# Kernel optimization log

Measured on AMD Instinct MI355X. Metric: run time of the kernel, lower is better.

The kernel has to match this reference:

```python
import jax, jax.numpy as jnp
import numpy as np

B, S, M = 2, 2048, 2048
NQ, NKV, H = 16, 4, 128
EPS = 1e-6
MAX_WAVELENGTH = 10000.0
NEG_INF = -1e9


def rmsnorm(x, scale, eps=EPS):
    # RMSNorm over head_dim (last axis), computed in fp32.
    xf = x.astype(jnp.float32)
    var = jnp.mean(xf * xf, axis=-1, keepdims=True)
    return (xf * jax.lax.rsqrt(var + eps) * scale).astype(x.dtype)


def rope(x, max_wavelength=MAX_WAVELENGTH, scaling_factor=1.0, start_index=0):
    # x: [b, s, n, h]; keras_hub split-half rotary embedding.
    h = x.shape[-1]
    inv_freq = 1.0 / (max_wavelength ** (jnp.arange(0, h, 2, dtype=jnp.float32) / h))
    pos = (jnp.arange(x.shape[1], dtype=jnp.float32) + start_index) / scaling_factor
    freq = pos[:, None] * inv_freq[None, :]             # [s, h/2]
    emb = jnp.concatenate([freq, freq], axis=-1)        # [s, h]
    cos = jnp.cos(emb)[None, :, None, :]
    sin = jnp.sin(emb)[None, :, None, :]
    x1, x2 = x[..., : h // 2], x[..., h // 2 :]
    rot = jnp.concatenate([-x2, x1], axis=-1)
    return (x * cos + rot * sin).astype(x.dtype)


def setup_inputs() -> dict:
    key = jax.random.key(0)
    ks = jax.random.split(key, 6)
    hidden_states = jax.random.normal(ks[0], (B, S, M), dtype=jnp.float32)
    # causal mask [b, q, k]
    causal = jnp.tril(jnp.ones((S, S), dtype=bool))
    attention_mask = jnp.broadcast_to(causal[None], (B, S, S))
    sq = 0.02
    Wq = jax.random.normal(ks[1], (M, NQ, H), dtype=jnp.float32) * sq
    Wk = jax.random.normal(ks[2], (M, NKV, H), dtype=jnp.float32) * sq
    Wv = jax.random.normal(ks[3], (M, NKV, H), dtype=jnp.float32) * sq
    Wo = jax.random.normal(ks[4], (NQ, H, M), dtype=jnp.float32) * sq
    q_scale = jnp.ones((H,), dtype=jnp.float32)
    k_scale = jnp.ones((H,), dtype=jnp.float32)
    return {
        "hidden_states": hidden_states,
        "attention_mask": attention_mask,
        "Wq": Wq,
        "Wk": Wk,
        "Wv": Wv,
        "Wo": Wo,
        "q_scale": q_scale,
        "k_scale": k_scale,
    }


def reference(hidden_states, attention_mask, Wq, Wk, Wv, Wo, q_scale, k_scale):
    inv_norm = 1.0 / np.sqrt(H)
    groups = NQ // NKV

    q = jnp.einsum("bqm,muh->bquh", hidden_states, Wq)   # [b,q,NQ,H]
    q = rope(rmsnorm(q, q_scale))
    k = jnp.einsum("bkm,mvh->bkvh", hidden_states, Wk)   # [b,k,NKV,H]
    k = rope(rmsnorm(k, k_scale))
    v = jnp.einsum("bkm,mvh->bkvh", hidden_states, Wv)

    # GQA broadcast: repeat each kv head `groups` times consecutively.
    k = jnp.repeat(k, groups, axis=2)
    v = jnp.repeat(v, groups, axis=2)

    scores = jnp.einsum("bquh,bkuh->buqk", q, k) * inv_norm  # [b,u,q,k]
    scores = scores.astype(jnp.float32)
    scores = jnp.where(attention_mask[:, None, :, :], scores, NEG_INF)
    probs = jax.nn.softmax(scores, axis=-1).astype(hidden_states.dtype)

    attn = jnp.einsum("buqk,bkuh->bquh", probs, v)
    out = jnp.einsum("bquh,uhm->bqm", attn, Wo)
    return out
```

## Files before the change

kernel.cpp:

```cpp
#include <hip/hip_runtime.h>
#include <stdint.h>

#define BB 2
#define SS 2048
#define MM 2048
#define NQ 16
#define NKV 4
#define HH 128
#define KVB 64

typedef __attribute__((ext_vector_type(4))) float f32x4;
typedef __attribute__((ext_vector_type(16))) float f32x16;
typedef _Float16 f16x8 __attribute__((ext_vector_type(8)));
typedef _Float16 f16x4 __attribute__((ext_vector_type(4)));
typedef _Float16 f16x2 __attribute__((ext_vector_type(2)));
typedef unsigned int uint4v __attribute__((ext_vector_type(4)));

__device__ __forceinline__ void gll16(const _Float16* g, _Float16* l) {
  __builtin_amdgcn_global_load_lds(
      (__attribute__((address_space(1))) void*)g,
      (__attribute__((address_space(3))) void*)l, 16, 0, 0);
}

__device__ __forceinline__ float fexp2(float x) {
#if __has_builtin(__builtin_amdgcn_exp2f)
  return __builtin_amdgcn_exp2f(x);
#else
  float r;
  asm("v_exp_f32 %0, %1" : "=v"(r) : "v"(x));
  return r;
#endif
}

__device__ __forceinline__ float fsin2pi(float rev) {
  float f, s;
  asm("v_fract_f32 %0, %1" : "=v"(f) : "v"(rev));
  asm("v_sin_f32 %0, %1" : "=v"(s) : "v"(f));
  return s;
}
__device__ __forceinline__ float fcos2pi(float rev) {
  float f, c;
  asm("v_fract_f32 %0, %1" : "=v"(f) : "v"(rev));
  asm("v_cos_f32 %0, %1" : "=v"(c) : "v"(f));
  return c;
}

__device__ __forceinline__ unsigned int pkrtz(float a, float b) {
  return __builtin_bit_cast(unsigned int, __builtin_amdgcn_cvt_pkrtz(a, b));
}

__global__ __launch_bounds__(256) void k_prep(
    const float* __restrict__ hidden,
    const float* __restrict__ Wq, const float* __restrict__ Wk,
    const float* __restrict__ Wv, const float* __restrict__ Wo,
    _Float16* __restrict__ Xb,
    _Float16* __restrict__ Wqkvt, _Float16* __restrict__ Wot) {
  const int z = blockIdx.z;
  if (z >= 4) {
    const int bid = (z - 4) * 4096 + blockIdx.y * 64 + blockIdx.x;
    const int i = bid * 256 + threadIdx.x;
    float4 v = ((const float4*)hidden)[i];
    f16x4 o = { (_Float16)v.x, (_Float16)v.y, (_Float16)v.z, (_Float16)v.w };
    ((f16x4*)Xb)[i] = o;
    return;
  }
  if (blockIdx.x >= 16) return;
  if ((z == 1 || z == 2) && blockIdx.y >= 16) return;
  const float* in = (z == 0) ? Wq : (z == 1) ? Wk : (z == 2) ? Wv : Wo;
  _Float16* out = (z == 3) ? Wot : Wqkvt;
  const int N_in = (z == 1 || z == 2) ? 512 : 2048;
  const int n_off = (z == 1) ? 2048 : (z == 2) ? 2560 : 0;

  __shared__ float tile[128][33];
  const int k0 = blockIdx.x * 128;
  const int n0 = blockIdx.y * 32;
  {
    const int rr = threadIdx.x >> 3;
    const int c4 = threadIdx.x & 7;
    #pragma unroll
    for (int it = 0; it < 4; ++it) {
      const int r = it * 32 + rr;
      const float4 v = *(const float4*)(&in[(size_t)(k0 + r) * N_in + n0 + c4 * 4]);
      tile[r][c4 * 4 + 0] = v.x;
      tile[r][c4 * 4 + 1] = v.y;
      tile[r][c4 * 4 + 2] = v.z;
      tile[r][c4 * 4 + 3] = v.w;
    }
  }
  __syncthreads();
  {
    const int rw = threadIdx.x >> 5;
    const int lk = threadIdx.x & 31;
    #pragma unroll
    for (int it = 0; it < 4; ++it) {
      const int r = it * 8 + rw;
      f16x4 o = { (_Float16)tile[lk * 4 + 0][r], (_Float16)tile[lk * 4 + 1][r],
                  (_Float16)tile[lk * 4 + 2][r], (_Float16)tile[lk * 4 + 3][r] };
      *(f16x4*)(&out[(size_t)(n0 + r + n_off) * 2048 + k0 + lk * 4]) = o;
    }
  }
}

template <int FN, bool F16OUT>
__global__ __launch_bounds__(512, 2) void k_gemm256(
    const _Float16* __restrict__ A, const _Float16* __restrict__ Bt,
    void* __restrict__ Cout, int NT_M, int N, int K) {
  __shared__ _Float16 As[2][256 * 64];
  __shared__ _Float16 Bs[2][FN * 64 * 64];

  const int tid = threadIdx.x;
  const int w = tid >> 6;
  const int l = tid & 63;
  const int lr = l & 15;
  const int al4 = l >> 4;
  const int wr = w >> 2;
  const int wc = w & 3;
  const int swz = (lr & 7) << 4;

  const int nwg = gridDim.x;
  const int bid = blockIdx.x;
  const int sbid = (bid & 7) * (nwg >> 3) + (bid >> 3);
  const int bm = (sbid % NT_M) * 256;
  const int bn = (sbid / NT_M) * (FN * 64);
  const int KT = K >> 6;

  const int srow = tid >> 3;
  const int sch = (tid & 7) ^ (srow & 7);
  const _Float16* aSrc = A + (size_t)(bm + srow) * K + sch * 8;
  const _Float16* bSrc = Bt + (size_t)(bn + srow) * K + sch * 8;

  auto stA = [&](int buf, int r, int kt) {
    gll16(aSrc + (size_t)(r * 64) * K + kt * 64, &As[buf][r * 4096 + w * 512]);
  };
  auto stB = [&](int buf, int r, int kt) {
    gll16(bSrc + (size_t)(r * 64) * K + kt * 64, &Bs[buf][r * 4096 + w * 512]);
  };

  f32x4 acc[8][FN] = {};

  stA(0, 0, 0); stA(0, 1, 0); stA(0, 2, 0); stA(0, 3, 0);
  stB(0, 0, 0); stB(0, 1, 0);
  if (FN == 3) stB(0, 2, 0);
  if (KT > 1) {
    stA(1, 0, 1); stA(1, 2, 1); stB(1, 0, 1); stB(1, 1, 1);
    asm volatile("s_waitcnt vmcnt(4)" ::: "memory");
  } else {
    asm volatile("s_waitcnt vmcnt(0)" ::: "memory");
  }
  __builtin_amdgcn_s_barrier();

  for (int t = 0; t < KT; ++t) {
    const int cb = t & 1;
    const char* Ab = (const char*)&As[cb][0];
    const char* Bb = (const char*)&Bs[cb][0];
    f16x8 bF[FN][2];
    #pragma unroll
    for (int ph = 0; ph < 2; ++ph) {
      f16x8 aF[4][2];
      #pragma unroll
      for (int fm = 0; fm < 4; ++fm)
        #pragma unroll
        for (int ks = 0; ks < 2; ++ks) {
          const int row = wr * 128 + (ph * 4 + fm) * 16 + lr;
          aF[fm][ks] = *(const f16x8*)(Ab + row * 128 + (((ks * 4 + al4) * 16) ^ swz));
        }
      if (ph == 0) {
        #pragma unroll
        for (int fn = 0; fn < FN; ++fn)
          #pragma unroll
          for (int ks = 0; ks < 2; ++ks) {
            const int col = wc * (FN * 16) + fn * 16 + lr;
            bF[fn][ks] = *(const f16x8*)(Bb + col * 128 + (((ks * 4 + al4) * 16) ^ swz));
          }
      }
      if (ph == 0 && t + 1 < KT) {
        if (FN == 3) stB(cb ^ 1, 2, t + 1);
        stA(cb ^ 1, 1, t + 1); stA(cb ^ 1, 3, t + 1);
      }
      if (ph == 1 && t + 2 < KT) {
        stA(cb, 0, t + 2); stA(cb, 2, t + 2);
        stB(cb, 0, t + 2); stB(cb, 1, t + 2);
      }
      __builtin_amdgcn_s_barrier();
      asm volatile("s_waitcnt lgkmcnt(0)" ::: "memory");
      __builtin_amdgcn_sched_barrier(0);
      __builtin_amdgcn_s_setprio(1);
      #pragma unroll
      for (int fm = 0; fm < 4; ++fm)
        #pragma unroll
        for (int fn = 0; fn < FN; ++fn)
          #pragma unroll
          for (int ks = 0; ks < 2; ++ks)
            acc[ph * 4 + fm][fn] = __builtin_amdgcn_mfma_f32_16x16x32_f16(
                aF[fm][ks], bF[fn][ks], acc[ph * 4 + fm][fn], 0, 0, 0);
      __builtin_amdgcn_s_setprio(0);
      __builtin_amdgcn_sched_barrier(0);
      if (ph == 0) {
        __builtin_amdgcn_s_barrier();
      } else {
        if (t + 2 < KT) asm volatile("s_waitcnt vmcnt(4)" ::: "memory");
        else            asm volatile("s_waitcnt vmcnt(0)" ::: "memory");
        __builtin_amdgcn_s_barrier();
      }
    }
  }

  #pragma unroll
  for (int fm = 0; fm < 8; ++fm) {
    #pragma unroll
    for (int i = 0; i < 4; ++i) {
      const int row = bm + wr * 128 + fm * 16 + al4 * 4 + i;
      #pragma unroll
      for (int fn = 0; fn < FN; ++fn) {
        const int col = bn + wc * (FN * 16) + fn * 16 + lr;
        if (F16OUT)
          ((_Float16*)Cout)[(size_t)row * N + col] = (_Float16)acc[fm][fn][i];
        else
          ((float*)Cout)[(size_t)row * N + col] = acc[fm][fn][i];
      }
    }
  }
}

__global__ __launch_bounds__(256) void k_normrope(
    const _Float16* __restrict__ qkv,
    const float* __restrict__ q_scale, const float* __restrict__ k_scale,
    _Float16* __restrict__ Qr, _Float16* __restrict__ Kr,
    _Float16* __restrict__ VtG) {
  __shared__ _Float16 vtile[32][33];
  if (blockIdx.y == 5) {
    if (blockIdx.x >= 2048) return;
    const int s0 = (blockIdx.x & 63) * 32;
    const int zz = blockIdx.x >> 6;
    const int h0 = (zz & 3) * 32;
    const int bv = zz >> 2;
    const int b = bv >> 2;
    const int hv = bv & 3;
    const int tx = threadIdx.x & 31;
    const int ty = threadIdx.x >> 5;
    #pragma unroll
    for (int r = ty; r < 32; r += 8)
      vtile[r][tx] = qkv[(size_t)(b * SS + s0 + r) * 3072 + 2560 + hv * 128 + h0 + tx];
    __syncthreads();
    #pragma unroll
    for (int r = ty; r < 32; r += 8)
      VtG[((size_t)bv * HH + h0 + r) * SS + s0 + tx] = vtile[tx][r];
    return;
  }
  const int row = blockIdx.x;
  const int b = row >> 11;
  const int s = row & 2047;
  const int hh = blockIdx.y * 4 + (threadIdx.x >> 6);
  const int l = threadIdx.x & 63;
  const _Float16* src = qkv + (size_t)row * 3072 + hh * 128 + l * 2;
  float x0 = (float)src[0];
  float x1 = (float)src[1];
  float ssum = x0 * x0 + x1 * x1;
  #pragma unroll
  for (int d = 1; d < 64; d <<= 1) ssum += __shfl_xor(ssum, d);
  const float rstd = rsqrtf(ssum * (1.f / 128.f) + 1e-6f);
  const float* scl = (hh < 16) ? q_scale : k_scale;
  x0 *= rstd * scl[2 * l];
  x1 *= rstd * scl[2 * l + 1];
  const float y0 = __shfl_xor(x0, 32);
  const float y1 = __shfl_xor(x1, 32);
  const int j0 = (2 * l) & 63;
  const float kLog = 0.20762050593046014f;
  const float inv2pi = 0.15915494309189535f;
  const float rev0 = (float)s * fexp2(-(float)j0 * kLog) * inv2pi;
  const float rev1 = (float)s * fexp2(-(float)(j0 + 1) * kLog) * inv2pi;
  const float c0 = fcos2pi(rev0), s0 = fsin2pi(rev0);
  const float c1 = fcos2pi(rev1), s1 = fsin2pi(rev1);
  float r0, r1;
  if (l < 32) { r0 = x0 * c0 - y0 * s0; r1 = x1 * c1 - y1 * s1; }
  else        { r0 = x0 * c0 + y0 * s0; r1 = x1 * c1 + y1 * s1; }
  if (hh < 16) {
    _Float16* dst = Qr + ((size_t)(b * NQ + hh) * SS + s) * HH + 2 * l;
    dst[0] = (_Float16)r0; dst[1] = (_Float16)r1;
  } else {
    _Float16* dst = Kr + ((size_t)(b * NKV + (hh - 16)) * SS + s) * HH + 2 * l;
    dst[0] = (_Float16)r0; dst[1] = (_Float16)r1;
  }
}

__device__ const unsigned char g_tasks[24] = {
  61, 63, 28,
  57, 59, 53, 55, 24,
  49, 51, 45, 47, 20,
  41, 43, 37, 39, 16,
  33, 35, 12,
  8, 4, 0
};

__global__ __launch_bounds__(256, 2) void k_attn(
    const _Float16* __restrict__ Qr, const _Float16* __restrict__ Kr,
    const _Float16* __restrict__ VtG,
    const float* __restrict__ qs, const float* __restrict__ ks,
    float* __restrict__ PartA, float* __restrict__ PartB,
    float* __restrict__ psA, float* __restrict__ psB,
    _Float16* __restrict__ Ao) {
  __shared__ _Float16 Ks[128 * 128];
  __shared__ _Float16 Vs[128 * 128];

  const int tid = threadIdx.x;
  const int w = tid >> 6;
  const int l = tid & 63;
  const int l31 = l & 31;
  const int hi = l >> 5;
  const int sw7 = (l31 & 7) << 4;

  const int n = blockIdx.y * 32 + blockIdx.x;
  const int g = n & 7;
  const int slot9 = n >> 3;
  const int j = slot9 & 3;
  const int b = g >> 2;
  const int kvh = g & 3;
  const int u = kvh * 4 + j;
  const int bu = b * 16 + u;

  const int task = g_tasks[slot9 >> 2];
  const int heavy = task & 1;
  const int half = (task >> 1) & 1;
  const int qt = task >> 2;
  const int q0 = qt * 128;
  const int total = 2 * qt + 2;
  const int h0 = ((qt + 2) >> 1) << 1;
  const int t0 = heavy ? (half ? h0 : 0) : 0;
  const int t1 = heavy ? (half ? total : h0) : total;

  float ma = fmaxf(fabsf(qs[l]), fabsf(qs[l + 64]));
  float mb = fmaxf(fabsf(ks[l]), fabsf(ks[l + 64]));
  #pragma unroll
  for (int d = 1; d < 64; d <<= 1) {
    ma = fmaxf(ma, __shfl_xor(ma, d));
    mb = fmaxf(mb, __shfl_xor(mb, d));
  }
  const float M2 = 1.4426950408889634f * ma * mb;
  const float K2 = 0.12752982260735795f;

  const _Float16* Kbase = Kr + (size_t)(b * NKV + kvh) * SS * HH;
  const _Float16* Vbase = VtG + (size_t)(b * NKV + kvh) * HH * SS;

  f16x8 qf[8];
  {
    const _Float16* qp = Qr + ((size_t)(b * NQ + u) * SS + q0 + w * 32 + l31) * HH + hi * 8;
    #pragma unroll
    for (int hs = 0; hs < 8; hs++) {
      qf[hs] = *(const f16x8*)(qp + hs * 16);
      qf[hs] *= (_Float16)K2;
    }
  }

  f32x16 acc0 = {}, acc1 = {}, acc2 = {}, acc3 = {};
  float psum = 0.f;

  auto stage = [&](int m) {
    const int kv0 = m * KVB;
    #pragma unroll
    for (int it = 0; it < 8; it++) {
      const int nn = it * 256 + tid;
      const int row = nn >> 4, c = nn & 15;
      const int cs = c ^ (row & 7);
      gll16(Kbase + (size_t)(kv0 + row) * HH + cs * 8,
            &Ks[(size_t)(it * 256 + w * 64) * 8]);
      gll16(Vbase + (size_t)row * SS + kv0 + cs * 8,
            &Vs[(size_t)(it * 256 + w * 64) * 8]);
    }
  };

  const int qwb = q0 + w * 32;
  const int qlane = qwb + l31;

  for (int m = t0; m < t1; m += 2) {
    stage(m);
    __syncthreads();
    const char* Kb = (const char*)&Ks[0];
    const char* Vb = (const char*)&Vs[0];
    #pragma unroll
    for (int hh2 = 0; hh2 < 2; ++hh2) {
      const int kv0 = m * KVB + hh2 * 64;
      if (kv0 <= qwb + 31) {
        f32x16 S0 = {}, S1 = {};
        __builtin_amdgcn_s_setprio(1);
        #pragma unroll
        for (int hs = 0; hs < 8; hs++) {
          const int ch = hs * 2 + hi;
          f16x8 k0 = *(const f16x8*)(Kb + (hh2 * 64 + l31) * 256 + ((ch << 4) ^ sw7));
          f16x8 k1 = *(const f16x8*)(Kb + (hh2 * 64 + 32 + l31) * 256 + ((ch << 4) ^ sw7));
          S0 = __builtin_amdgcn_mfma_f32_32x32x16_f16(k0, qf[hs], S0, 0, 0, 0);
          S1 = __builtin_amdgcn_mfma_f32_32x32x16_f16(k1, qf[hs], S1, 0, 0, 0);
        }
        __builtin_amdgcn_s_setprio(0);

        const bool domask = (kv0 + 63 > qwb);
        float p0[16], p1[16];
        #pragma unroll
        for (int r = 0; r < 16; r++) {
          const int cr = (r & 3) + 8 * (r >> 2) + 4 * hi;
          float e0 = fexp2(S0[r] - M2);
          float e1 = fexp2(S1[r] - M2);
          if (domask) {
            if (kv0 + cr > qlane) e0 = 0.f;
            if (kv0 + 32 + cr > qlane) e1 = 0.f;
          }
          p0[r] = e0; p1[r] = e1;
          psum += e0 + e1;
        }

        unsigned int pkv[4][4];
        #pragma unroll
        for (int gg = 0; gg < 4; gg++) {
          pkv[0][gg] = pkrtz(p0[2 * gg], p0[2 * gg + 1]);
          pkv[1][gg] = pkrtz(p0[8 + 2 * gg], p0[9 + 2 * gg]);
          pkv[2][gg] = pkrtz(p1[2 * gg], p1[2 * gg + 1]);
          pkv[3][gg] = pkrtz(p1[8 + 2 * gg], p1[9 + 2 * gg]);
        }
        f16x8 pa[4];
        #pragma unroll
        for (int ksx = 0; ksx < 4; ksx++) {
          unsigned int a0 = pkv[ksx][0], a1 = pkv[ksx][1], a2 = pkv[ksx][2], a3 = pkv[ksx][3];
          unsigned int x0 = (unsigned int)__shfl_xor((int)a0, 32);
          unsigned int x1 = (unsigned int)__shfl_xor((int)a1, 32);
          unsigned int x2 = (unsigned int)__shfl_xor((int)a2, 32);
          unsigned int x3 = (unsigned int)__shfl_xor((int)a3, 32);
          uint4v dv;
          dv.x = hi ? x2 : a0;
          dv.y = hi ? x3 : a1;
          dv.z = hi ? a2 : x0;
          dv.w = hi ? a3 : x1;
          pa[ksx] = __builtin_bit_cast(f16x8, dv);
        }

        __builtin_amdgcn_s_setprio(1);
        #pragma unroll
        for (int ksx = 0; ksx < 4; ksx++) {
          const int ch = hh2 * 8 + ksx * 2 + hi;
          f16x8 v0 = *(const f16x8*)(Vb + (0 * 32 + l31) * 256 + ((ch << 4) ^ sw7));
          acc0 = __builtin_amdgcn_mfma_f32_32x32x16_f16(pa[ksx], v0, acc0, 0, 0, 0);
          f16x8 v1 = *(const f16x8*)(Vb + (1 * 32 + l31) * 256 + ((ch << 4) ^ sw7));
          acc1 = __builtin_amdgcn_mfma_f32_32x32x16_f16(pa[ksx], v1, acc1, 0, 0, 0);
          f16x8 v2 = *(const f16x8*)(Vb + (2 * 32 + l31) * 256 + ((ch << 4) ^ sw7));
          acc2 = __builtin_amdgcn_mfma_f32_32x32x16_f16(pa[ksx], v2, acc2, 0, 0, 0);
          f16x8 v3 = *(const f16x8*)(Vb + (3 * 32 + l31) * 256 + ((ch << 4) ^ sw7));
          acc3 = __builtin_amdgcn_mfma_f32_32x32x16_f16(pa[ksx], v3, acc3, 0, 0, 0);
        }
        __builtin_amdgcn_s_setprio(0);
      }
    }
    __syncthreads();
  }

  const float tot = psum + __shfl_xor(psum, 32);
  if (heavy) {
    const int slot = bu * 8 + (qt - 8);
    float* pPart = (half ? PartB : PartA) + (size_t)slot * 16384;
    float* sPart = (half ? psB : psA) + slot * 128;
    if (hi == 0) sPart[w * 32 + l31] = tot;
    #pragma unroll
    for (int r = 0; r < 16; r++) {
      const int cr = (r & 3) + 8 * (r >> 2) + 4 * hi;
      float* dst = pPart + (size_t)(w * 32 + cr) * 128 + l31;
      dst[0]  = acc0[r];
      dst[32] = acc1[r];
      dst[64] = acc2[r];
      dst[96] = acc3[r];
    }
  } else {
    const float inv = 1.f / tot;
    #pragma unroll
    for (int r = 0; r < 16; r++) {
      const int cr = (r & 3) + 8 * (r >> 2) + 4 * hi;
      const float ivr = __shfl(inv, cr);
      _Float16* dst = Ao + ((size_t)(b * SS + q0 + w * 32 + cr)) * MM + u * HH + l31;
      dst[0]  = (_Float16)(acc0[r] * ivr);
      dst[32] = (_Float16)(acc1[r] * ivr);
      dst[64] = (_Float16)(acc2[r] * ivr);
      dst[96] = (_Float16)(acc3[r] * ivr);
    }
  }
}

__global__ __launch_bounds__(256) void k_fin(
    const float* __restrict__ PartA, const float* __restrict__ PartB,
    const float* __restrict__ psA, const float* __restrict__ psB,
    _Float16* __restrict__ Ao) {
  const int slot = blockIdx.x;
  const int bu = slot >> 3, st = slot & 7;
  const int b = bu >> 4, u = bu & 15;
  const int qt = st + 8;
  const float* pa = PartA + (size_t)slot * 16384;
  const float* pb = PartB + (size_t)slot * 16384;
  const float* sa = psA + slot * 128;
  const float* sb = psB + slot * 128;
  #pragma unroll
  for (int it = 0; it < 16; it++) {
    const int unit = it * 256 + threadIdx.x;
    const int qr = unit >> 5, cg = unit & 31;
    const float inv = 1.f / (sa[qr] + sb[qr]);
    f32x4 va = *(const f32x4*)(pa + qr * 128 + cg * 4);
    f32x4 vb = *(const f32x4*)(pb + qr * 128 + cg * 4);
    f16x4 o = { (_Float16)((va[0] + vb[0]) * inv), (_Float16)((va[1] + vb[1]) * inv),
                (_Float16)((va[2] + vb[2]) * inv), (_Float16)((va[3] + vb[3]) * inv) };
    *(f16x4*)(Ao + ((size_t)(b * SS + qt * 128 + qr)) * MM + u * HH + cg * 4) = o;
  }
}

extern "C" void kernel_launch(void* const* d_in, const int* in_sizes, int n_in,
                              void* d_out, int out_size, void* d_ws, size_t ws_size,
                              hipStream_t stream) {
  const float* hidden = (const float*)d_in[0];
  const float* Wq = (const float*)d_in[2];
  const float* Wk = (const float*)d_in[3];
  const float* Wv = (const float*)d_in[4];
  const float* Wo = (const float*)d_in[5];
  const float* q_scale = (const float*)d_in[6];
  const float* k_scale = (const float*)d_in[7];

  char* ws = (char*)d_ws;
  _Float16* Xb    = (_Float16*)(ws);
  _Float16* Wqkvt = (_Float16*)(ws + 16777216);
  _Float16* Wot   = (_Float16*)(ws + 29360128);
  _Float16* qkv   = (_Float16*)(ws + 37748736);
  _Float16* Qr    = (_Float16*)(ws + 62914560);
  _Float16* Kr    = (_Float16*)(ws + 79691776);
  _Float16* VtG   = (_Float16*)(ws + 83886080);
  _Float16* Ao    = (_Float16*)(ws + 88080384);
  float*    PartB = (float*)(ws);
  float*    PartA = (float*)(ws + 37748736);
  float*    psA   = (float*)(ws + 54525952);
  float*    psB   = (float*)(ws + 54657024);

  k_prep<<<dim3(64, 64, 6), dim3(256), 0, stream>>>(hidden, Wq, Wk, Wv, Wo, Xb, Wqkvt, Wot);
  k_gemm256<3, true><<<dim3(256), dim3(512), 0, stream>>>(Xb, Wqkvt, (void*)qkv, 16, 3072, 2048);
  k_normrope<<<dim3(4096, 6), dim3(256), 0, stream>>>(qkv, q_scale, k_scale, Qr, Kr, VtG);
  k_attn<<<dim3(32, 24), dim3(256), 0, stream>>>(Qr, Kr, VtG, q_scale, k_scale,
                                                 PartA, PartB, psA, psB, Ao);
  k_fin<<<dim3(256), dim3(256), 0, stream>>>(PartA, PartB, psA, psB, Ao);
  k_gemm256<2, false><<<dim3(256), dim3(512), 0, stream>>>(Ao, Wot, d_out, 16, 2048, 2048);
}
```

Before: 193.7 us.

## Shrink GEMM N-tile to 128, single-buffer B tile, raise occupancy target

The GEMM kernel now uses a fixed 256x128 output tile instead of the 256x192 tile used for the QKV projection, so that GEMM launches 384 blocks instead of 256. The B tile in LDS drops from double to single buffering: the next B tile is loaded in the second phase, after every wave has pulled its B fragments into registers. The launch bounds now ask for 4 blocks per CU, with vmcnt waits adjusted to match. The aim is better load balance across CUs and less LDS per block. The risks are register spilling under the tighter bound, since LDS use per block still probably allows only about 2 blocks per CU, and a B load that is less well hidden.

```diff
diff --git a/kernel.cpp b/kernel.cpp
--- a/kernel.cpp
+++ b/kernel.cpp
@@ -101,12 +101,12 @@
   }
 }
 
-template <int FN, bool F16OUT>
-__global__ __launch_bounds__(512, 2) void k_gemm256(
+template <bool F16OUT>
+__global__ __launch_bounds__(512, 4) void k_gemm256(
     const _Float16* __restrict__ A, const _Float16* __restrict__ Bt,
     void* __restrict__ Cout, int NT_M, int N, int K) {
   __shared__ _Float16 As[2][256 * 64];
-  __shared__ _Float16 Bs[2][FN * 64 * 64];
+  __shared__ _Float16 Bs[128 * 64];
 
   const int tid = threadIdx.x;
   const int w = tid >> 6;
@@ -121,7 +121,7 @@
   const int bid = blockIdx.x;
   const int sbid = (bid & 7) * (nwg >> 3) + (bid >> 3);
   const int bm = (sbid % NT_M) * 256;
-  const int bn = (sbid / NT_M) * (FN * 64);
+  const int bn = (sbid / NT_M) * 128;
   const int KT = K >> 6;
 
   const int srow = tid >> 3;
@@ -132,18 +132,17 @@
   auto stA = [&](int buf, int r, int kt) {
     gll16(aSrc + (size_t)(r * 64) * K + kt * 64, &As[buf][r * 4096 + w * 512]);
   };
-  auto stB = [&](int buf, int r, int kt) {
-    gll16(bSrc + (size_t)(r * 64) * K + kt * 64, &Bs[buf][r * 4096 + w * 512]);
+  auto stB = [&](int r, int kt) {
+    gll16(bSrc + (size_t)(r * 64) * K + kt * 64, &Bs[r * 4096 + w * 512]);
   };
 
-  f32x4 acc[8][FN] = {};
+  f32x4 acc[8][2] = {};
 
   stA(0, 0, 0); stA(0, 1, 0); stA(0, 2, 0); stA(0, 3, 0);
-  stB(0, 0, 0); stB(0, 1, 0);
-  if (FN == 3) stB(0, 2, 0);
+  stB(0, 0); stB(1, 0);
   if (KT > 1) {
-    stA(1, 0, 1); stA(1, 2, 1); stB(1, 0, 1); stB(1, 1, 1);
-    asm volatile("s_waitcnt vmcnt(4)" ::: "memory");
+    stA(1, 0, 1); stA(1, 2, 1);
+    asm volatile("s_waitcnt vmcnt(2)" ::: "memory");
   } else {
     asm volatile("s_waitcnt vmcnt(0)" ::: "memory");
   }
@@ -152,8 +151,8 @@
   for (int t = 0; t < KT; ++t) {
     const int cb = t & 1;
     const char* Ab = (const char*)&As[cb][0];
-    const char* Bb = (const char*)&Bs[cb][0];
-    f16x8 bF[FN][2];
+    const char* Bb = (const char*)&Bs[0];
+    f16x8 bF[2][2];
     #pragma unroll
     for (int ph = 0; ph < 2; ++ph) {
       f16x8 aF[4][2];
@@ -166,20 +165,19 @@
         }
       if (ph == 0) {
         #pragma unroll
-        for (int fn = 0; fn < FN; ++fn)
+        for (int fn = 0; fn < 2; ++fn)
           #pragma unroll
           for (int ks = 0; ks < 2; ++ks) {
-            const int col = wc * (FN * 16) + fn * 16 + lr;
+            const int col = wc * 32 + fn * 16 + lr;
             bF[fn][ks] = *(const f16x8*)(Bb + col * 128 + (((ks * 4 + al4) * 16) ^ swz));
           }
       }
       if (ph == 0 && t + 1 < KT) {
-        if (FN == 3) stB(cb ^ 1, 2, t + 1);
         stA(cb ^ 1, 1, t + 1); stA(cb ^ 1, 3, t + 1);
       }
-      if (ph == 1 && t + 2 < KT) {
-        stA(cb, 0, t + 2); stA(cb, 2, t + 2);
-        stB(cb, 0, t + 2); stB(cb, 1, t + 2);
+      if (ph == 1) {
+        if (t + 1 < KT) { stB(0, t + 1); stB(1, t + 1); }
+        if (t + 2 < KT) { stA(cb, 0, t + 2); stA(cb, 2, t + 2); }
       }
       __builtin_amdgcn_s_barrier();
       asm volatile("s_waitcnt lgkmcnt(0)" ::: "memory");
@@ -188,7 +186,7 @@
       #pragma unroll
       for (int fm = 0; fm < 4; ++fm)
         #pragma unroll
-        for (int fn = 0; fn < FN; ++fn)
+        for (int fn = 0; fn < 2; ++fn)
           #pragma unroll
           for (int ks = 0; ks < 2; ++ks)
             acc[ph * 4 + fm][fn] = __builtin_amdgcn_mfma_f32_16x16x32_f16(
@@ -198,7 +196,7 @@
       if (ph == 0) {
         __builtin_amdgcn_s_barrier();
       } else {
-        if (t + 2 < KT) asm volatile("s_waitcnt vmcnt(4)" ::: "memory");
+        if (t + 2 < KT) asm volatile("s_waitcnt vmcnt(2)" ::: "memory");
         else            asm volatile("s_waitcnt vmcnt(0)" ::: "memory");
         __builtin_amdgcn_s_barrier();
       }
@@ -211,8 +209,8 @@
     for (int i = 0; i < 4; ++i) {
       const int row = bm + wr * 128 + fm * 16 + al4 * 4 + i;
       #pragma unroll
-      for (int fn = 0; fn < FN; ++fn) {
-        const int col = bn + wc * (FN * 16) + fn * 16 + lr;
+      for (int fn = 0; fn < 2; ++fn) {
+        const int col = bn + wc * 32 + fn * 16 + lr;
         if (F16OUT)
           ((_Float16*)Cout)[(size_t)row * N + col] = (_Float16)acc[fm][fn][i];
         else
@@ -531,10 +529,10 @@
   float*    psB   = (float*)(ws + 54657024);
 
   k_prep<<<dim3(64, 64, 6), dim3(256), 0, stream>>>(hidden, Wq, Wk, Wv, Wo, Xb, Wqkvt, Wot);
-  k_gemm256<3, true><<<dim3(256), dim3(512), 0, stream>>>(Xb, Wqkvt, (void*)qkv, 16, 3072, 2048);
+  k_gemm256<true><<<dim3(384), dim3(512), 0, stream>>>(Xb, Wqkvt, (void*)qkv, 16, 3072, 2048);
   k_normrope<<<dim3(4096, 6), dim3(256), 0, stream>>>(qkv, q_scale, k_scale, Qr, Kr, VtG);
   k_attn<<<dim3(32, 24), dim3(256), 0, stream>>>(Qr, Kr, VtG, q_scale, k_scale,
                                                  PartA, PartB, psA, psB, Ao);
   k_fin<<<dim3(256), dim3(256), 0, stream>>>(PartA, PartB, psA, psB, Ao);
-  k_gemm256<2, false><<<dim3(256), dim3(512), 0, stream>>>(Ao, Wot, d_out, 16, 2048, 2048);
-}
+  k_gemm256<false><<<dim3(256), dim3(512), 0, stream>>>(Ao, Wot, d_out, 16, 2048, 2048);
+}
```

Result: slower. 330.5 us (+70.6%).
